# Performance work log

Measured on AMD Instinct MI355X. Metric: run time of the kernel, lower is better.

The kernel has to match this reference:

```python
import jax, jax.numpy as jnp
import numpy as np

C = 2.0 + 1e-6
_nodes, _weights = np.polynomial.laguerre.laggauss(2)
QUAD_NODES = jnp.asarray(np.maximum(_nodes, 0.01) / C, dtype=jnp.float32)
QUAD_WEIGHTS = jnp.asarray(np.maximum(_weights, 0.01) / C, dtype=jnp.float32)
H, HD, P, M = 4, 64, 16, 32  # heads, head_dim, poly_dim, num_features
NUM_LABELS = 131072


def safe_normalize(x, axis=-1, eps=1e-4):
    n = jnp.linalg.norm(x, axis=axis, keepdims=True)
    return x / jnp.maximum(n, eps)


def safe_log(x, eps=1e-8):
    return jnp.log(jnp.maximum(x, eps))


def slay_features(x, omega, anchors):
    # x: [N, H*HD]; omega: [R,H,HD,M] (pre-scaled); anchors: [P,HD] (unit-norm)
    N = x.shape[0]
    xr = safe_normalize(x.reshape(N, H, HD), axis=-1)
    poly_proj = jnp.clip(jnp.einsum('nhd,pd->nhp', xr, anchors), -1.0, 1.0)
    poly_feat = poly_proj ** 2 / np.float32(np.sqrt(P))          # [N,H,P]
    prf_proj = jnp.einsum('nhd,rhdm->rnhm', xr, omega)           # [R,N,H,M]
    s = jnp.maximum(QUAD_NODES, 1e-6).reshape(-1, 1, 1, 1)
    exp_arg = jnp.clip(prf_proj * jnp.sqrt(2.0 * s) - s, -20.0, 20.0)
    prf_feat = jnp.exp(exp_arg) / np.float32(np.sqrt(M + 1e-6))
    prf_feat = prf_feat * jnp.sqrt(jnp.maximum(QUAD_WEIGHTS, 1e-6)).reshape(-1, 1, 1, 1)
    # fuse poly x prf, concat over quadrature nodes r (r-major feature order)
    fused = poly_feat[None, :, :, :, None] * prf_feat[:, :, :, None, :]  # [R,N,H,P,M]
    return fused.transpose(1, 0, 2, 3, 4).reshape(N, -1)         # [N, R*H*P*M]


def setup_inputs() -> dict:
    key = jax.random.key(0)
    ks = jax.random.split(key, 9)
    B, L, K = 1024, 128, 8
    return {
        'indices': jax.random.randint(ks[0], (B, L), 0, 100000),
        'mask': jnp.ones((B, L), dtype=jnp.float32),
        'labels': jax.random.randint(ks[1], (B, K), 0, NUM_LABELS),
        'label_mask': jnp.ones((B, K), dtype=jnp.float32),
        'neg_indices': jax.random.randint(ks[2], (2048,), 0, NUM_LABELS),
        'embed_table': jax.random.normal(ks[3], (100000, 256), dtype=jnp.float32),
        'kernel': jax.random.normal(ks[4], (256, NUM_LABELS), dtype=jnp.float32),
        'omega': jax.random.normal(ks[5], (2, H, HD, M), dtype=jnp.float32),
        'anchors': jax.random.normal(ks[6], (P, HD), dtype=jnp.float32),
    }


def reference(indices, mask, labels, label_mask, neg_indices, embed_table, kernel, omega, anchors):
    B, K = labels.shape
    # init-time parameter normalizations from the module
    omega_n = omega / np.float32(np.sqrt(HD))
    anchors_n = anchors / jnp.linalg.norm(anchors, axis=-1, keepdims=True)
    # MeanEmbedding encoder
    embeds = embed_table[indices]                                 # [B,L,D]
    summed = jnp.sum(embeds * mask[:, :, None], axis=1)
    query = summed / jnp.maximum(jnp.sum(mask, axis=1, keepdims=True), 1.0)
    query = safe_normalize(query, axis=-1)
    phi_query = slay_features(query, omega_n, anchors_n)          # [B,F]
    # sampled classifier rows
    W = safe_normalize(kernel.T, axis=-1)                         # [num_labels,D]
    safe_labels = jnp.maximum(labels, 0)
    all_needed = jnp.concatenate([safe_labels.reshape(-1), neg_indices])  # [B*K+Nneg]
    W_subset = W[all_needed]
    phi_W = slay_features(W_subset, omega_n, anchors_n)           # [B*K+Nneg,F]
    scores = phi_query @ phi_W.T                                  # [B, B*K+Nneg]
    idx_offsets = jnp.arange(B)[:, None] * K + jnp.arange(K)[None, :]
    pos_scores = jnp.take_along_axis(scores, idx_offsets, axis=1) # [B,K]
    neg_scores = scores[:, B * K:]                                # [B,Nneg]
    all_scores = jnp.concatenate([pos_scores, neg_scores], axis=1) + 1e-8
    log_Z = jax.scipy.special.logsumexp(safe_log(all_scores), axis=1)
    log_probs = safe_log(pos_scores + 1e-8) - log_Z[:, None]
    return -jnp.sum(log_probs * label_mask) / (jnp.sum(label_mask) + 1e-6)
```

## Files before the change

kernel.cpp:

```cpp
#include <hip/hip_runtime.h>
#include <math.h>

#define B_Q 1024
#define L_SEQ 128
#define D_EMB 256
#define NLAB 131072
#define LBL_ROWS 8192
#define NEG_ROWS 2048
#define W_ROWS 10240
#define CROW 320
#define LST 82
#define RPB 8

__device__ __forceinline__ float wave_sum(float v) {
#pragma unroll
  for (int off = 32; off > 0; off >>= 1) v += __shfl_xor(v, off, 64);
  return v;
}

__device__ __forceinline__ void slay_tail(const float* __restrict__ sx, int t,
                                          const float* __restrict__ anchT,
                                          const float* __restrict__ omega,
                                          float* __restrict__ outrow) {
  if (t < 64) {
    const int h = t >> 4, p = t & 15;
    const float* x = sx + h * 64;
    float d = 0.f;
#pragma unroll
    for (int dd = 0; dd < 64; dd++) d = fmaf(x[dd], anchT[dd * 16 + p], d);
    d = fminf(fmaxf(d, -1.0f), 1.0f);
    outrow[h * 16 + p] = d * d * 0.25f;
  }
  {
    const int r = t >> 7, h = (t >> 5) & 3;
    const float* x = sx + h * 64;
    const float* om = omega + (size_t)(t >> 5) * 2048 + (t & 31);
    float d = 0.f;
#pragma unroll
    for (int dd = 0; dd < 64; dd++) d = fmaf(x[dd], om[dd * 32], d);
    const float proj = d * 0.125f;
    const float s = r ? 1.70710592763316f : 0.29289307236691f;
    const float w = r ? 0.07322326809171f : 0.42677648190829f;
    float arg = proj * sqrtf(2.0f * s) - s;
    arg = fminf(fmaxf(arg, -20.0f), 20.0f);
    outrow[64 + t] = expf(arg) * (sqrtf(w) / sqrtf(32.000001f));
  }
}

__global__ __launch_bounds__(256) void k_prep(const float* __restrict__ anchors,
                                              float* __restrict__ anchT,
                                              float* __restrict__ negparts) {
  const int t = threadIdx.x;
  if (blockIdx.x == 0) {
    if (t < 64) {
      for (int p = 0; p < 16; p++) {
        const float v = anchors[p * 64 + t];
        const float n = sqrtf(wave_sum(v * v));
        anchT[t * 16 + p] = v / n;
      }
    }
  } else {
    negparts[(blockIdx.x - 1) * 256 + t] = 0.f;
  }
}

__global__ __launch_bounds__(256) void k_query(const int* __restrict__ indices,
                                               const float* __restrict__ mask,
                                               const float* __restrict__ embed,
                                               const float* __restrict__ anchT,
                                               const float* __restrict__ omega,
                                               float* __restrict__ qcomp) {
  const int b = blockIdx.x, t = threadIdx.x;
  const int wv = t >> 6, ln = t & 63;
  __shared__ int sidx[L_SEQ];
  __shared__ float smask[L_SEQ];
  __shared__ float4 spart[256];
  __shared__ float smsum[4];
  __shared__ float sx[256];
  if (t < L_SEQ) { sidx[t] = indices[b * L_SEQ + t]; smask[t] = mask[b * L_SEQ + t]; }
  __syncthreads();
  float4 acc = {0.f, 0.f, 0.f, 0.f};
  float msum = 0.f;
#pragma unroll 8
  for (int l = wv * 32; l < wv * 32 + 32; l++) {
    const float m = smask[l];
    msum += m;
    const float4 e = *(const float4*)(embed + (size_t)sidx[l] * D_EMB + ln * 4);
    acc.x = fmaf(e.x, m, acc.x); acc.y = fmaf(e.y, m, acc.y);
    acc.z = fmaf(e.z, m, acc.z); acc.w = fmaf(e.w, m, acc.w);
  }
  spart[wv * 64 + ln] = acc;
  if (ln == 0) smsum[wv] = msum;
  __syncthreads();
  const float* spf = (const float*)spart;
  float q = spf[t] + spf[256 + t] + spf[512 + t] + spf[768 + t];
  const float mt = smsum[0] + smsum[1] + smsum[2] + smsum[3];
  q /= fmaxf(mt, 1.0f);
  const float ss = wave_sum(q * q);
  sx[t] = q / fmaxf(sqrtf(ss), 1e-4f);
  __syncthreads();
  slay_tail(sx, t, anchT, omega, qcomp + (size_t)b * CROW);
}

__global__ __launch_bounds__(256) void k_wrows(const int* __restrict__ labels,
                                               const int* __restrict__ negidx,
                                               const float* __restrict__ kern,
                                               const float* __restrict__ anchT,
                                               const float* __restrict__ omega,
                                               float* __restrict__ wcomp) {
  __shared__ int sj[RPB];
  __shared__ float sx[RPB * 256];
  __shared__ float snorm[RPB * 4];
  const int tid = threadIdx.x;
  const int i0 = blockIdx.x * RPB;

  if (tid < RPB) {
    const int i = i0 + tid;
    int j;
    if (i < LBL_ROWS) { j = labels[i]; if (j < 0) j = 0; }
    else               { j = negidx[i - LBL_ROWS]; }
    sj[tid] = j;
  }
  __syncthreads();

#pragma unroll
  for (int k = 0; k < RPB; k++) {
    const int idx = k * 256 + tid;
    sx[idx] = kern[(size_t)(idx & 255) * NLAB + sj[idx >> 8]];
  }
  __syncthreads();

  {
    const int row = tid >> 5, sub = tid & 31;
    const float* xp = sx + row * 256 + sub * 8;
    float ssum = 0.f;
#pragma unroll
    for (int e = 0; e < 8; e++) ssum = fmaf(xp[e], xp[e], ssum);
    ssum += __shfl_xor(ssum, 1, 64);
    ssum += __shfl_xor(ssum, 2, 64);
    ssum += __shfl_xor(ssum, 4, 64);
    if ((sub & 7) == 0) snorm[row * 4 + (sub >> 3)] = fmaxf(sqrtf(ssum), 1e-4f);
  }
  __syncthreads();
#pragma unroll
  for (int k = 0; k < RPB; k++) {
    const int idx = k * 256 + tid;
    sx[idx] /= snorm[(idx >> 8) * 4 + ((idx >> 6) & 3)];
  }
  __syncthreads();

  {
    const int h = (tid >> 5) & 3, r = tid >> 7;
    const float* om = omega + (size_t)(tid >> 5) * 2048 + (tid & 31);
    float acc[RPB];
#pragma unroll
    for (int row = 0; row < RPB; row++) acc[row] = 0.f;
#pragma unroll
    for (int dd = 0; dd < 64; dd += 2) {
      const float o0 = om[dd * 32], o1 = om[dd * 32 + 32];
#pragma unroll
      for (int row = 0; row < RPB; row++) {
        const float2 xv = *(const float2*)(sx + row * 256 + h * 64 + dd);
        acc[row] = fmaf(xv.x, o0, fmaf(xv.y, o1, acc[row]));
      }
    }
    const float s = r ? 1.70710592763316f : 0.29289307236691f;
    const float w = r ? 0.07322326809171f : 0.42677648190829f;
    const float sc = sqrtf(2.0f * s);
    const float outs = sqrtf(w) / sqrtf(32.000001f);
#pragma unroll
    for (int row = 0; row < RPB; row++) {
      float arg = acc[row] * 0.125f * sc - s;
      arg = fminf(fmaxf(arg, -20.0f), 20.0f);
      wcomp[(size_t)(i0 + row) * CROW + 64 + tid] = expf(arg) * outs;
    }
  }

  {
    const int hp = tid & 63, rp = tid >> 6;
    const int h = hp >> 4, p = hp & 15;
    const float* x0 = sx + (rp * 2) * 256 + h * 64;
    const float* x1 = x0 + 256;
    float d0 = 0.f, d1 = 0.f;
#pragma unroll
    for (int dd = 0; dd < 64; dd++) {
      const float a = anchT[dd * 16 + p];
      d0 = fmaf(x0[dd], a, d0);
      d1 = fmaf(x1[dd], a, d1);
    }
    d0 = fminf(fmaxf(d0, -1.0f), 1.0f);
    d1 = fminf(fmaxf(d1, -1.0f), 1.0f);
    wcomp[(size_t)(i0 + rp * 2) * CROW + h * 16 + p]     = d0 * d0 * 0.25f;
    wcomp[(size_t)(i0 + rp * 2 + 1) * CROW + h * 16 + p] = d1 * d1 * 0.25f;
  }
}

__global__ __launch_bounds__(128) void k_neg(const float* __restrict__ qcomp,
                                             const float* __restrict__ wcomp,
                                             float* __restrict__ negparts) {
  __shared__ float qt[64 * LST];
  __shared__ float wt[32 * LST];
  const int tid = threadIdx.x;
  const int qb0 = blockIdx.x * 64;
  const int wr0 = LBL_ROWS + blockIdx.y * 32;
  const int h = blockIdx.z;

  for (int idx = tid; idx < 96 * 20; idx += 128) {
    const int row = idx / 20, c4 = idx % 20;
    int col, lcol;
    if (c4 < 4)       { col = h * 16 + c4 * 4;              lcol = c4 * 4; }
    else if (c4 < 12) { col = 64 + h * 32 + (c4 - 4) * 4;   lcol = 16 + (c4 - 4) * 4; }
    else              { col = 192 + h * 32 + (c4 - 12) * 4; lcol = 48 + (c4 - 12) * 4; }
    const bool isq = row < 64;
    const int grow = isq ? (qb0 + row) : (wr0 + row - 64);
    const float4 v = *(const float4*)((isq ? qcomp : wcomp) + (size_t)grow * CROW + col);
    float* dst = (isq ? qt + row * LST : wt + (row - 64) * LST) + lcol;
    dst[0] = v.x; dst[1] = v.y; dst[2] = v.z; dst[3] = v.w;
  }
  __syncthreads();

  const int qg = tid >> 3;
  const int wg = tid & 7;
  const float* qb = qt + (qg * 4) * LST;
  const float* wb = wt + (wg * 4) * LST;

  float pd[4][4] = {{0.f}}, pf[4][4] = {{0.f}};
#pragma unroll
  for (int kc = 0; kc < 8; kc++) {
    float2 qv[4], wv[4];
#pragma unroll
    for (int i = 0; i < 4; i++) qv[i] = *(const float2*)(qb + i * LST + 2 * kc);
#pragma unroll
    for (int j = 0; j < 4; j++) wv[j] = *(const float2*)(wb + j * LST + 2 * kc);
#pragma unroll
    for (int i = 0; i < 4; i++)
#pragma unroll
      for (int j = 0; j < 4; j++) {
        pd[i][j] = fmaf(qv[i].x, wv[j].x, pd[i][j]);
        pd[i][j] = fmaf(qv[i].y, wv[j].y, pd[i][j]);
      }
  }
#pragma unroll 8
  for (int kc = 0; kc < 32; kc++) {
    float2 qv[4], wv[4];
#pragma unroll
    for (int i = 0; i < 4; i++) qv[i] = *(const float2*)(qb + i * LST + 16 + 2 * kc);
#pragma unroll
    for (int j = 0; j < 4; j++) wv[j] = *(const float2*)(wb + j * LST + 16 + 2 * kc);
#pragma unroll
    for (int i = 0; i < 4; i++)
#pragma unroll
      for (int j = 0; j < 4; j++) {
        pf[i][j] = fmaf(qv[i].x, wv[j].x, pf[i][j]);
        pf[i][j] = fmaf(qv[i].y, wv[j].y, pf[i][j]);
      }
  }

#pragma unroll
  for (int i = 0; i < 4; i++) {
    float acc = 0.f;
#pragma unroll
    for (int j = 0; j < 4; j++) acc += pd[i][j] * pf[i][j];
#pragma unroll
    for (int off = 1; off < 8; off <<= 1) acc += __shfl_xor(acc, off, 64);
    if (wg == 0) atomicAdd(&negparts[blockIdx.y * B_Q + qb0 + qg * 4 + i], acc);
  }
}

__global__ __launch_bounds__(256) void k_pos(const float* __restrict__ qcomp,
                                             const float* __restrict__ wcomp,
                                             float* __restrict__ pos) {
  const int tid = threadIdx.x;
  const int g = blockIdx.x * 64 + (tid >> 2);
  const int h = tid & 3;
  const float* q = qcomp + (size_t)(g >> 3) * CROW;
  const float* w = wcomp + (size_t)g * CROW;
  float pd = 0.f, pf = 0.f;
#pragma unroll
  for (int c = 0; c < 4; c++) {
    const float4 qv = *(const float4*)(q + h * 16 + c * 4);
    const float4 wv = *(const float4*)(w + h * 16 + c * 4);
    pd += qv.x * wv.x + qv.y * wv.y + qv.z * wv.z + qv.w * wv.w;
  }
#pragma unroll
  for (int r = 0; r < 2; r++)
#pragma unroll
    for (int c = 0; c < 8; c++) {
      const float4 qv = *(const float4*)(q + 64 + r * 128 + h * 32 + c * 4);
      const float4 wv = *(const float4*)(w + 64 + r * 128 + h * 32 + c * 4);
      pf += qv.x * wv.x + qv.y * wv.y + qv.z * wv.z + qv.w * wv.w;
    }
  float sc = pd * pf;
  sc += __shfl_xor(sc, 1, 64);
  sc += __shfl_xor(sc, 2, 64);
  if (h == 0) pos[g] = sc;
}

__global__ __launch_bounds__(1024) void k_loss(const float* __restrict__ pos,
                                               const float* __restrict__ negparts,
                                               const float* __restrict__ lmask,
                                               float* __restrict__ out) {
  const int b = threadIdx.x;
  float lp[8];
  float possum = 0.f;
#pragma unroll
  for (int k = 0; k < 8; k++) { lp[k] = pos[b * 8 + k]; possum += lp[k]; }
  float negsum = 0.f;
#pragma unroll 8
  for (int c = 0; c < 64; c++) negsum += negparts[c * B_Q + b];
  const float Z = possum + negsum + 2.056e-5f;
  const float logZ = logf(Z);
  float local = 0.f, lsum = 0.f;
#pragma unroll
  for (int k = 0; k < 8; k++) {
    const float lm = lmask[b * 8 + k];
    local += lm * (logf(lp[k] + 1e-8f) - logZ);
    lsum += lm;
  }
  local = wave_sum(local);
  lsum = wave_sum(lsum);
  __shared__ float r1[16], r2[16];
  const int wid = b >> 6;
  if ((b & 63) == 0) { r1[wid] = local; r2[wid] = lsum; }
  __syncthreads();
  if (b == 0) {
    float t1 = 0.f, t2 = 0.f;
    for (int wv = 0; wv < 16; wv++) { t1 += r1[wv]; t2 += r2[wv]; }
    out[0] = -t1 / (t2 + 1e-6f);
  }
}

extern "C" void kernel_launch(void* const* d_in, const int* in_sizes, int n_in,
                              void* d_out, int out_size, void* d_ws, size_t ws_size,
                              hipStream_t stream) {
  const int* indices  = (const int*)d_in[0];
  const float* mask   = (const float*)d_in[1];
  const int* labels   = (const int*)d_in[2];
  const float* lmask  = (const float*)d_in[3];
  const int* negidx   = (const int*)d_in[4];
  const float* embed  = (const float*)d_in[5];
  const float* kern   = (const float*)d_in[6];
  const float* omega  = (const float*)d_in[7];
  const float* anchors= (const float*)d_in[8];
  float* out = (float*)d_out;

  float* ws = (float*)d_ws;
  float* anchT    = ws;
  float* qcomp    = anchT + 1024;
  float* wcomp    = qcomp + (size_t)B_Q * CROW;
  float* pos      = wcomp + (size_t)W_ROWS * CROW;
  float* negparts = pos + LBL_ROWS;

  k_prep<<<257, 256, 0, stream>>>(anchors, anchT, negparts);
  k_query<<<B_Q, 256, 0, stream>>>(indices, mask, embed, anchT, omega, qcomp);
  k_wrows<<<W_ROWS / RPB, 256, 0, stream>>>(labels, negidx, kern, anchT, omega, wcomp);
  k_neg<<<dim3(16, 64, 4), 128, 0, stream>>>(qcomp, wcomp, negparts);
  k_pos<<<128, 256, 0, stream>>>(qcomp, wcomp, pos);
  k_loss<<<1, 1024, 0, stream>>>(pos, negparts, lmask, out);
}
```

Measured before the change: 361.8 us.

## Stream kernel matrix column-wise with claim map instead of strided gathers; enlarge neg tile

Replaces the per-row strided gather of classifier columns with a pass that streams the whole kernel matrix in coalesced column chunks. A claim table marks which label columns are needed, only claimed columns are staged in shared memory for feature computation, and a fix-up kernel copies features to rows that reference duplicate columns. This trades uncoalesced scattered reads for a full coalesced read of the 128 MB matrix. The negative-score kernel is also retiled to 64 W rows per block with float4 shared loads, which halves the number of partial sums.

Result: slower. 784.5 us (+116.8%).

```diff
diff --git a/kernel.cpp b/kernel.cpp
--- a/kernel.cpp
+++ b/kernel.cpp
@@ -9,8 +9,10 @@
 #define NEG_ROWS 2048
 #define W_ROWS 10240
 #define CROW 320
-#define LST 82
-#define RPB 8
+#define LSTN 84
+#define WCH 256
+#define WNB 44
+#define WLS 258
 
 __device__ __forceinline__ float wave_sum(float v) {
 #pragma unroll
@@ -49,9 +51,10 @@
 
 __global__ __launch_bounds__(256) void k_prep(const float* __restrict__ anchors,
                                               float* __restrict__ anchT,
-                                              float* __restrict__ negparts) {
-  const int t = threadIdx.x;
-  if (blockIdx.x == 0) {
+                                              float* __restrict__ negparts,
+                                              int* __restrict__ claim) {
+  const int t = threadIdx.x, bx = blockIdx.x;
+  if (bx == 0) {
     if (t < 64) {
       for (int p = 0; p < 16; p++) {
         const float v = anchors[p * 64 + t];
@@ -59,9 +62,24 @@
         anchT[t * 16 + p] = v / n;
       }
     }
+  } else if (bx <= 128) {
+    negparts[(bx - 1) * 256 + t] = 0.f;
   } else {
-    negparts[(blockIdx.x - 1) * 256 + t] = 0.f;
-  }
+    claim[(bx - 129) * 256 + t] = -1;
+  }
+}
+
+__global__ __launch_bounds__(256) void k_mark(const int* __restrict__ labels,
+                                              const int* __restrict__ negidx,
+                                              int* __restrict__ claim,
+                                              int* __restrict__ jidx) {
+  const int i = blockIdx.x * 256 + threadIdx.x;
+  if (i >= W_ROWS) return;
+  int j;
+  if (i < LBL_ROWS) { j = labels[i]; if (j < 0) j = 0; }
+  else               { j = negidx[i - LBL_ROWS]; }
+  claim[j] = i;
+  jidx[i] = j;
 }
 
 __global__ __launch_bounds__(256) void k_query(const int* __restrict__ indices,
@@ -102,110 +120,128 @@
   slay_tail(sx, t, anchT, omega, qcomp + (size_t)b * CROW);
 }
 
-__global__ __launch_bounds__(256) void k_wrows(const int* __restrict__ labels,
-                                               const int* __restrict__ negidx,
-                                               const float* __restrict__ kern,
-                                               const float* __restrict__ anchT,
-                                               const float* __restrict__ omega,
-                                               float* __restrict__ wcomp) {
-  __shared__ int sj[RPB];
-  __shared__ float sx[RPB * 256];
-  __shared__ float snorm[RPB * 4];
+__global__ __launch_bounds__(256) void k_wstage(const float* __restrict__ kern,
+                                                const int* __restrict__ claim,
+                                                const float* __restrict__ anchT,
+                                                const float* __restrict__ omega,
+                                                float* __restrict__ wcomp) {
+  __shared__ __align__(16) float sx[48 * WLS];
+  __shared__ float snorm[WNB * 4];
+  __shared__ int lcol2a[WCH];
+  __shared__ int lowner[WCH];
+  __shared__ int scnt;
   const int tid = threadIdx.x;
-  const int i0 = blockIdx.x * RPB;
-
-  if (tid < RPB) {
-    const int i = i0 + tid;
-    int j;
-    if (i < LBL_ROWS) { j = labels[i]; if (j < 0) j = 0; }
-    else               { j = negidx[i - LBL_ROWS]; }
-    sj[tid] = j;
-  }
-  __syncthreads();
-
-#pragma unroll
-  for (int k = 0; k < RPB; k++) {
-    const int idx = k * 256 + tid;
-    sx[idx] = kern[(size_t)(idx & 255) * NLAB + sj[idx >> 8]];
-  }
-  __syncthreads();
-
-  {
-    const int row = tid >> 5, sub = tid & 31;
-    const float* xp = sx + row * 256 + sub * 8;
-    float ssum = 0.f;
-#pragma unroll
-    for (int e = 0; e < 8; e++) ssum = fmaf(xp[e], xp[e], ssum);
-    ssum += __shfl_xor(ssum, 1, 64);
-    ssum += __shfl_xor(ssum, 2, 64);
-    ssum += __shfl_xor(ssum, 4, 64);
-    if ((sub & 7) == 0) snorm[row * 4 + (sub >> 3)] = fmaxf(sqrtf(ssum), 1e-4f);
-  }
-  __syncthreads();
-#pragma unroll
-  for (int k = 0; k < RPB; k++) {
-    const int idx = k * 256 + tid;
-    sx[idx] /= snorm[(idx >> 8) * 4 + ((idx >> 6) & 3)];
-  }
-  __syncthreads();
-
-  {
-    const int h = (tid >> 5) & 3, r = tid >> 7;
-    const float* om = omega + (size_t)(tid >> 5) * 2048 + (tid & 31);
-    float acc[RPB];
-#pragma unroll
-    for (int row = 0; row < RPB; row++) acc[row] = 0.f;
-#pragma unroll
-    for (int dd = 0; dd < 64; dd += 2) {
-      const float o0 = om[dd * 32], o1 = om[dd * 32 + 32];
-#pragma unroll
-      for (int row = 0; row < RPB; row++) {
-        const float2 xv = *(const float2*)(sx + row * 256 + h * 64 + dd);
-        acc[row] = fmaf(xv.x, o0, fmaf(xv.y, o1, acc[row]));
-      }
-    }
-    const float s = r ? 1.70710592763316f : 0.29289307236691f;
-    const float w = r ? 0.07322326809171f : 0.42677648190829f;
-    const float sc = sqrtf(2.0f * s);
-    const float outs = sqrtf(w) / sqrtf(32.000001f);
-#pragma unroll
-    for (int row = 0; row < RPB; row++) {
-      float arg = acc[row] * 0.125f * sc - s;
-      arg = fminf(fmaxf(arg, -20.0f), 20.0f);
-      wcomp[(size_t)(i0 + row) * CROW + 64 + tid] = expf(arg) * outs;
-    }
-  }
-
-  {
-    const int hp = tid & 63, rp = tid >> 6;
-    const int h = hp >> 4, p = hp & 15;
-    const float* x0 = sx + (rp * 2) * 256 + h * 64;
-    const float* x1 = x0 + 256;
-    float d0 = 0.f, d1 = 0.f;
-#pragma unroll
-    for (int dd = 0; dd < 64; dd++) {
-      const float a = anchT[dd * 16 + p];
-      d0 = fmaf(x0[dd], a, d0);
-      d1 = fmaf(x1[dd], a, d1);
-    }
-    d0 = fminf(fmaxf(d0, -1.0f), 1.0f);
-    d1 = fminf(fmaxf(d1, -1.0f), 1.0f);
-    wcomp[(size_t)(i0 + rp * 2) * CROW + h * 16 + p]     = d0 * d0 * 0.25f;
-    wcomp[(size_t)(i0 + rp * 2 + 1) * CROW + h * 16 + p] = d1 * d1 * 0.25f;
+  const int c0 = blockIdx.x * WCH;
+  if (tid == 0) scnt = 0;
+  lcol2a[tid] = -1;
+  __syncthreads();
+  const int owner = claim[c0 + tid];
+  int mya = -1;
+  if (owner >= 0) { mya = atomicAdd(&scnt, 1); lcol2a[tid] = mya; lowner[mya] = owner; }
+  __syncthreads();
+  const int cnt = scnt;
+  float cs = 0.f;
+  const size_t colbase = (size_t)(c0 + tid);
+
+  for (int bs = 0; bs < cnt; bs += WNB) {
+    const int nb = min(WNB, cnt - bs);
+    __syncthreads();
+    const int aloc = (mya >= bs && mya < bs + nb) ? (mya - bs) : -1;
+    for (int t = 0; t < 256; t += 8) {
+      float v[8];
+#pragma unroll
+      for (int k = 0; k < 8; k++) v[k] = kern[(size_t)(t + k) * NLAB + colbase];
+#pragma unroll
+      for (int k = 0; k < 8; k++) cs += v[k];
+      if (aloc >= 0) {
+#pragma unroll
+        for (int k = 0; k < 8; k++) sx[aloc * WLS + t + k] = v[k];
+      }
+    }
+    __syncthreads();
+    for (int a = tid >> 5; a < nb; a += 8) {
+      const int sub = tid & 31;
+      const float* xp = sx + a * WLS + sub * 8;
+      float ssum = 0.f;
+#pragma unroll
+      for (int e = 0; e < 8; e++) ssum = fmaf(xp[e], xp[e], ssum);
+      ssum += __shfl_xor(ssum, 1, 64);
+      ssum += __shfl_xor(ssum, 2, 64);
+      ssum += __shfl_xor(ssum, 4, 64);
+      if ((sub & 7) == 0) snorm[a * 4 + (sub >> 3)] = fmaxf(sqrtf(ssum), 1e-4f);
+    }
+    __syncthreads();
+    for (int idx = tid; idx < nb * 256; idx += 256)
+      sx[(idx >> 8) * WLS + (idx & 255)] /= snorm[(idx >> 8) * 4 + ((idx >> 6) & 3)];
+    __syncthreads();
+    {
+      const int h = (tid >> 5) & 3, r = tid >> 7;
+      const float* om = omega + (size_t)(tid >> 5) * 2048 + (tid & 31);
+      const float s = r ? 1.70710592763316f : 0.29289307236691f;
+      const float w = r ? 0.07322326809171f : 0.42677648190829f;
+      const float sc = sqrtf(2.0f * s);
+      const float outs = sqrtf(w) / sqrtf(32.000001f);
+      for (int rb = 0; rb < nb; rb += 8) {
+        float acc[8] = {0.f, 0.f, 0.f, 0.f, 0.f, 0.f, 0.f, 0.f};
+#pragma unroll
+        for (int dd = 0; dd < 64; dd += 2) {
+          const float o0 = om[dd * 32], o1 = om[dd * 32 + 32];
+#pragma unroll
+          for (int rr = 0; rr < 8; rr++) {
+            const float2 xv = *(const float2*)(sx + (rb + rr) * WLS + h * 64 + dd);
+            acc[rr] = fmaf(xv.x, o0, fmaf(xv.y, o1, acc[rr]));
+          }
+        }
+#pragma unroll
+        for (int rr = 0; rr < 8; rr++) {
+          if (rb + rr < nb) {
+            float arg = fminf(fmaxf(acc[rr] * 0.125f * sc - s, -20.f), 20.f);
+            wcomp[(size_t)lowner[bs + rb + rr] * CROW + 64 + tid] = expf(arg) * outs;
+          }
+        }
+      }
+    }
+    {
+      const int hp = tid & 63, rg = tid >> 6;
+      const int h = hp >> 4, p = hp & 15;
+      for (int row = rg; row < nb; row += 4) {
+        const float* x = sx + row * WLS + h * 64;
+        float d = 0.f;
+#pragma unroll
+        for (int dd = 0; dd < 64; dd++) d = fmaf(x[dd], anchT[dd * 16 + p], d);
+        d = fminf(fmaxf(d, -1.0f), 1.0f);
+        wcomp[(size_t)lowner[bs + row] * CROW + h * 16 + p] = d * d * 0.25f;
+      }
+    }
+  }
+  if (cnt > 255) sx[0] = cs;
+}
+
+__global__ __launch_bounds__(256) void k_fix(const int* __restrict__ claim,
+                                             const int* __restrict__ jidx,
+                                             float* __restrict__ wcomp) {
+  const int i = (blockIdx.x * 256 + threadIdx.x) >> 6;
+  const int lane = threadIdx.x & 63;
+  const int j = jidx[i];
+  const int own = claim[j];
+  if (own != i) {
+#pragma unroll
+    for (int l = 0; l < 5; l++)
+      wcomp[(size_t)i * CROW + lane + 64 * l] = wcomp[(size_t)own * CROW + lane + 64 * l];
   }
 }
 
 __global__ __launch_bounds__(128) void k_neg(const float* __restrict__ qcomp,
                                              const float* __restrict__ wcomp,
                                              float* __restrict__ negparts) {
-  __shared__ float qt[64 * LST];
-  __shared__ float wt[32 * LST];
+  __shared__ __align__(16) float qt[64 * LSTN];
+  __shared__ __align__(16) float wt[64 * LSTN];
   const int tid = threadIdx.x;
   const int qb0 = blockIdx.x * 64;
-  const int wr0 = LBL_ROWS + blockIdx.y * 32;
+  const int wr0 = LBL_ROWS + blockIdx.y * 64;
   const int h = blockIdx.z;
 
-  for (int idx = tid; idx < 96 * 20; idx += 128) {
+  for (int idx = tid; idx < 128 * 20; idx += 128) {
     const int row = idx / 20, c4 = idx % 20;
     int col, lcol;
     if (c4 < 4)       { col = h * 16 + c4 * 4;              lcol = c4 * 4; }
@@ -214,56 +250,59 @@
     const bool isq = row < 64;
     const int grow = isq ? (qb0 + row) : (wr0 + row - 64);
     const float4 v = *(const float4*)((isq ? qcomp : wcomp) + (size_t)grow * CROW + col);
-    float* dst = (isq ? qt + row * LST : wt + (row - 64) * LST) + lcol;
-    dst[0] = v.x; dst[1] = v.y; dst[2] = v.z; dst[3] = v.w;
-  }
-  __syncthreads();
-
-  const int qg = tid >> 3;
-  const int wg = tid & 7;
-  const float* qb = qt + (qg * 4) * LST;
-  const float* wb = wt + (wg * 4) * LST;
-
-  float pd[4][4] = {{0.f}}, pf[4][4] = {{0.f}};
-#pragma unroll
-  for (int kc = 0; kc < 8; kc++) {
-    float2 qv[4], wv[4];
-#pragma unroll
-    for (int i = 0; i < 4; i++) qv[i] = *(const float2*)(qb + i * LST + 2 * kc);
-#pragma unroll
-    for (int j = 0; j < 4; j++) wv[j] = *(const float2*)(wb + j * LST + 2 * kc);
-#pragma unroll
-    for (int i = 0; i < 4; i++)
+    *(float4*)((isq ? qt + row * LSTN : wt + (row - 64) * LSTN) + lcol) = v;
+  }
+  __syncthreads();
+
+  const int qg = tid >> 4;
+  const int wg = tid & 15;
+  float pd[8][4] = {{0.f}}, pf[8][4] = {{0.f}};
+
+#pragma unroll
+  for (int kc = 0; kc < 4; kc++) {
+    float4 qv[8], wv[4];
+#pragma unroll
+    for (int i = 0; i < 8; i++) qv[i] = *(const float4*)(qt + (qg + 8 * i) * LSTN + kc * 4);
+#pragma unroll
+    for (int j = 0; j < 4; j++) wv[j] = *(const float4*)(wt + (wg + 16 * j) * LSTN + kc * 4);
+#pragma unroll
+    for (int i = 0; i < 8; i++)
 #pragma unroll
       for (int j = 0; j < 4; j++) {
         pd[i][j] = fmaf(qv[i].x, wv[j].x, pd[i][j]);
         pd[i][j] = fmaf(qv[i].y, wv[j].y, pd[i][j]);
-      }
-  }
-#pragma unroll 8
-  for (int kc = 0; kc < 32; kc++) {
-    float2 qv[4], wv[4];
-#pragma unroll
-    for (int i = 0; i < 4; i++) qv[i] = *(const float2*)(qb + i * LST + 16 + 2 * kc);
-#pragma unroll
-    for (int j = 0; j < 4; j++) wv[j] = *(const float2*)(wb + j * LST + 16 + 2 * kc);
-#pragma unroll
-    for (int i = 0; i < 4; i++)
+        pd[i][j] = fmaf(qv[i].z, wv[j].z, pd[i][j]);
+        pd[i][j] = fmaf(qv[i].w, wv[j].w, pd[i][j]);
+      }
+  }
+#pragma unroll
+  for (int kc = 4; kc < 20; kc++) {
+    float4 qv[8], wv[4];
+#pragma unroll
+    for (int i = 0; i < 8; i++) qv[i] = *(const float4*)(qt + (qg + 8 * i) * LSTN + kc * 4);
+#pragma unroll
+    for (int j = 0; j < 4; j++) wv[j] = *(const float4*)(wt + (wg + 16 * j) * LSTN + kc * 4);
+#pragma unroll
+    for (int i = 0; i < 8; i++)
 #pragma unroll
       for (int j = 0; j < 4; j++) {
         pf[i][j] = fmaf(qv[i].x, wv[j].x, pf[i][j]);
         pf[i][j] = fmaf(qv[i].y, wv[j].y, pf[i][j]);
-      }
-  }
-
-#pragma unroll
-  for (int i = 0; i < 4; i++) {
+        pf[i][j] = fmaf(qv[i].z, wv[j].z, pf[i][j]);
+        pf[i][j] = fmaf(qv[i].w, wv[j].w, pf[i][j]);
+      }
+  }
+
+#pragma unroll
+  for (int i = 0; i < 8; i++) {
     float acc = 0.f;
 #pragma unroll
     for (int j = 0; j < 4; j++) acc += pd[i][j] * pf[i][j];
-#pragma unroll
-    for (int off = 1; off < 8; off <<= 1) acc += __shfl_xor(acc, off, 64);
-    if (wg == 0) atomicAdd(&negparts[blockIdx.y * B_Q + qb0 + qg * 4 + i], acc);
+    acc += __shfl_xor(acc, 1, 64);
+    acc += __shfl_xor(acc, 2, 64);
+    acc += __shfl_xor(acc, 4, 64);
+    acc += __shfl_xor(acc, 8, 64);
+    if (wg == 0) atomicAdd(&negparts[blockIdx.y * B_Q + qb0 + qg + 8 * i], acc);
   }
 }
 
@@ -307,7 +346,7 @@
   for (int k = 0; k < 8; k++) { lp[k] = pos[b * 8 + k]; possum += lp[k]; }
   float negsum = 0.f;
 #pragma unroll 8
-  for (int c = 0; c < 64; c++) negsum += negparts[c * B_Q + b];
+  for (int c = 0; c < 32; c++) negsum += negparts[c * B_Q + b];
   const float Z = possum + negsum + 2.056e-5f;
   const float logZ = logf(Z);
   float local = 0.f, lsum = 0.f;
@@ -350,11 +389,15 @@
   float* wcomp    = qcomp + (size_t)B_Q * CROW;
   float* pos      = wcomp + (size_t)W_ROWS * CROW;
   float* negparts = pos + LBL_ROWS;
-
-  k_prep<<<257, 256, 0, stream>>>(anchors, anchT, negparts);
+  int*   claim    = (int*)(negparts + 32 * B_Q);
+  int*   jidx     = claim + NLAB;
+
+  k_prep<<<641, 256, 0, stream>>>(anchors, anchT, negparts, claim);
+  k_mark<<<40, 256, 0, stream>>>(labels, negidx, claim, jidx);
   k_query<<<B_Q, 256, 0, stream>>>(indices, mask, embed, anchT, omega, qcomp);
-  k_wrows<<<W_ROWS / RPB, 256, 0, stream>>>(labels, negidx, kern, anchT, omega, wcomp);
-  k_neg<<<dim3(16, 64, 4), 128, 0, stream>>>(qcomp, wcomp, negparts);
+  k_wstage<<<NLAB / WCH, 256, 0, stream>>>(kern, claim, anchT, omega, wcomp);
+  k_fix<<<W_ROWS / 4, 256, 0, stream>>>(claim, jidx, wcomp);
+  k_neg<<<dim3(16, 32, 4), 128, 0, stream>>>(qcomp, wcomp, negparts);
   k_pos<<<128, 256, 0, stream>>>(qcomp, wcomp, pos);
   k_loss<<<1, 1024, 0, stream>>>(pos, negparts, lmask, out);
 }
```

## Counting-sort gathered label columns by 64-column bucket to coalesce kernel reads

Applied to the files above, without the earlier changes.

Adds a bucket histogram, scan and scatter pass that orders the 10240 requested kernel columns by column index in groups of 64. k_wrows then processes rows in that sorted order and remaps its block index so blocks running at the same time touch nearby columns of the strided 256x131072 kernel matrix. The aim is to improve cache-line reuse for the column gather, which reads one float per 512 KB stride. The cost is three extra small kernel launches with atomics, plus scattered writes to wcomp.

Measured after the change: 358.3 us. Within noise of the previous version (-1.0%).

```diff
diff --git a/kernel.cpp b/kernel.cpp
--- a/kernel.cpp
+++ b/kernel.cpp
@@ -49,9 +49,10 @@
 
 __global__ __launch_bounds__(256) void k_prep(const float* __restrict__ anchors,
                                               float* __restrict__ anchT,
-                                              float* __restrict__ negparts) {
-  const int t = threadIdx.x;
-  if (blockIdx.x == 0) {
+                                              float* __restrict__ negparts,
+                                              int* __restrict__ hist) {
+  const int t = threadIdx.x, bx = blockIdx.x;
+  if (bx == 0) {
     if (t < 64) {
       for (int p = 0; p < 16; p++) {
         const float v = anchors[p * 64 + t];
@@ -59,9 +60,52 @@
         anchT[t * 16 + p] = v / n;
       }
     }
+  } else if (bx <= 256) {
+    negparts[(bx - 1) * 256 + t] = 0.f;
   } else {
-    negparts[(blockIdx.x - 1) * 256 + t] = 0.f;
-  }
+    hist[(bx - 257) * 256 + t] = 0;
+  }
+}
+
+__global__ __launch_bounds__(256) void k_mark(const int* __restrict__ labels,
+                                              const int* __restrict__ negidx,
+                                              int* __restrict__ jidx,
+                                              int* __restrict__ hist) {
+  const int i = blockIdx.x * 256 + threadIdx.x;
+  if (i >= W_ROWS) return;
+  int j;
+  if (i < LBL_ROWS) { j = labels[i]; if (j < 0) j = 0; }
+  else               { j = negidx[i - LBL_ROWS]; }
+  jidx[i] = j;
+  atomicAdd(&hist[j >> 6], 1);
+}
+
+__global__ __launch_bounds__(256) void k_scan(int* __restrict__ hist) {
+  __shared__ int s[256];
+  const int t = threadIdx.x;
+  int v[8]; int sum = 0;
+#pragma unroll
+  for (int e = 0; e < 8; e++) { v[e] = hist[t * 8 + e]; sum += v[e]; }
+  s[t] = sum; __syncthreads();
+  for (int off = 1; off < 256; off <<= 1) {
+    const int x = s[t];
+    const int y = (t >= off) ? s[t - off] : 0;
+    __syncthreads();
+    s[t] = x + y;
+    __syncthreads();
+  }
+  int run = s[t] - sum;
+#pragma unroll
+  for (int e = 0; e < 8; e++) { hist[t * 8 + e] = run; run += v[e]; }
+}
+
+__global__ __launch_bounds__(256) void k_scatter(const int* __restrict__ jidx,
+                                                 int* __restrict__ hist,
+                                                 int* __restrict__ sorted) {
+  const int i = blockIdx.x * 256 + threadIdx.x;
+  if (i >= W_ROWS) return;
+  const int pos = atomicAdd(&hist[jidx[i] >> 6], 1);
+  sorted[pos] = i;
 }
 
 __global__ __launch_bounds__(256) void k_query(const int* __restrict__ indices,
@@ -102,24 +146,24 @@
   slay_tail(sx, t, anchT, omega, qcomp + (size_t)b * CROW);
 }
 
-__global__ __launch_bounds__(256) void k_wrows(const int* __restrict__ labels,
-                                               const int* __restrict__ negidx,
+__global__ __launch_bounds__(256) void k_wrows(const int* __restrict__ sorted,
+                                               const int* __restrict__ jidx,
                                                const float* __restrict__ kern,
                                                const float* __restrict__ anchT,
                                                const float* __restrict__ omega,
                                                float* __restrict__ wcomp) {
   __shared__ int sj[RPB];
+  __shared__ int ssid[RPB];
   __shared__ float sx[RPB * 256];
   __shared__ float snorm[RPB * 4];
   const int tid = threadIdx.x;
-  const int i0 = blockIdx.x * RPB;
+  const int cb = (blockIdx.x & 7) * 160 + (blockIdx.x >> 3);
+  const int i0 = cb * RPB;
 
   if (tid < RPB) {
-    const int i = i0 + tid;
-    int j;
-    if (i < LBL_ROWS) { j = labels[i]; if (j < 0) j = 0; }
-    else               { j = negidx[i - LBL_ROWS]; }
-    sj[tid] = j;
+    const int sid = sorted[i0 + tid];
+    ssid[tid] = sid;
+    sj[tid] = jidx[sid];
   }
   __syncthreads();
 
@@ -172,7 +216,7 @@
     for (int row = 0; row < RPB; row++) {
       float arg = acc[row] * 0.125f * sc - s;
       arg = fminf(fmaxf(arg, -20.0f), 20.0f);
-      wcomp[(size_t)(i0 + row) * CROW + 64 + tid] = expf(arg) * outs;
+      wcomp[(size_t)ssid[row] * CROW + 64 + tid] = expf(arg) * outs;
     }
   }
 
@@ -190,8 +234,8 @@
     }
     d0 = fminf(fmaxf(d0, -1.0f), 1.0f);
     d1 = fminf(fmaxf(d1, -1.0f), 1.0f);
-    wcomp[(size_t)(i0 + rp * 2) * CROW + h * 16 + p]     = d0 * d0 * 0.25f;
-    wcomp[(size_t)(i0 + rp * 2 + 1) * CROW + h * 16 + p] = d1 * d1 * 0.25f;
+    wcomp[(size_t)ssid[rp * 2] * CROW + h * 16 + p]     = d0 * d0 * 0.25f;
+    wcomp[(size_t)ssid[rp * 2 + 1] * CROW + h * 16 + p] = d1 * d1 * 0.25f;
   }
 }
 
@@ -350,10 +394,16 @@
   float* wcomp    = qcomp + (size_t)B_Q * CROW;
   float* pos      = wcomp + (size_t)W_ROWS * CROW;
   float* negparts = pos + LBL_ROWS;
-
-  k_prep<<<257, 256, 0, stream>>>(anchors, anchT, negparts);
+  int*   jidx     = (int*)(negparts + 64 * B_Q);
+  int*   sorted   = jidx + W_ROWS;
+  int*   hist     = sorted + W_ROWS;
+
+  k_prep<<<265, 256, 0, stream>>>(anchors, anchT, negparts, hist);
+  k_mark<<<40, 256, 0, stream>>>(labels, negidx, jidx, hist);
+  k_scan<<<1, 256, 0, stream>>>(hist);
+  k_scatter<<<40, 256, 0, stream>>>(jidx, hist, sorted);
   k_query<<<B_Q, 256, 0, stream>>>(indices, mask, embed, anchT, omega, qcomp);
-  k_wrows<<<W_ROWS / RPB, 256, 0, stream>>>(labels, negidx, kern, anchT, omega, wcomp);
+  k_wrows<<<W_ROWS / RPB, 256, 0, stream>>>(sorted, jidx, kern, anchT, omega, wcomp);
   k_neg<<<dim3(16, 64, 4), 128, 0, stream>>>(qcomp, wcomp, negparts);
   k_pos<<<128, 256, 0, stream>>>(qcomp, wcomp, pos);
   k_loss<<<1, 1024, 0, stream>>>(pos, negparts, lmask, out);
```
